# Kernel tuning notes

Measured on AMD Instinct MI355X. Metric: run time of the kernel, lower is better.

Reference implementation:

```python
import jax, jax.numpy as jnp
import numpy as np

N, C, H, O, NUM_CLASSES = 4096, 768, 512, 50, 1


def setup_inputs() -> dict:
    key = jax.random.key(0)
    ks = jax.random.split(key, 8)
    x = jax.random.normal(ks[0], (N, C), dtype=jnp.float32)
    labels = jax.random.randint(ks[1], (N,), 0, 2, dtype=jnp.int64)
    W1 = jax.random.normal(ks[2], (C, H), dtype=jnp.float32) / np.sqrt(C)
    b1 = jnp.zeros((H,), dtype=jnp.float32)
    W2 = jax.random.normal(ks[3], (H, O), dtype=jnp.float32) / np.sqrt(H)
    b2 = jnp.zeros((O,), dtype=jnp.float32)
    fcW = jax.random.normal(ks[4], (C + O, NUM_CLASSES), dtype=jnp.float32) / np.sqrt(C + O)
    fcb = jnp.zeros((NUM_CLASSES,), dtype=jnp.float32)
    return {"x": x, "labels": labels, "W1": W1, "b1": b1, "W2": W2, "b2": b2, "fcW": fcW, "fcb": fcb}


def _build_graph(x, labels):
    # similarity-threshold edge construction (dense masked form of the python double loop)
    sim = x @ x.T                                   # [N, N]
    n = x.shape[0]
    diff = labels[:, None] != labels[None, :]       # cross-label pairs
    cnt = jnp.sum(diff)
    s = jnp.sum(jnp.where(diff, sim, 0.0))
    threshold = jnp.where(cnt > 0, s / cnt.astype(sim.dtype), jnp.asarray(0.0, sim.dtype))
    eye = jnp.eye(n, dtype=bool)
    same = (labels[:, None] == labels[None, :]) & ~eye
    edge_mask = same & (sim <= threshold)           # symmetric (sim symmetric)
    loss_mask = edge_mask & (jnp.arange(n)[:, None] < jnp.arange(n)[None, :])  # i<j pairs
    adj = jax.lax.stop_gradient(edge_mask.astype(x.dtype))
    # GCN normalization with self-loops
    a = adj + jnp.eye(n, dtype=x.dtype)
    dinv = jax.lax.rsqrt(jnp.sum(a, axis=1))        # deg >= 1
    norm_adj = dinv[:, None] * a * dinv[None, :]
    return norm_adj, loss_mask


def reference(x, labels, W1, b1, W2, b2, fcW, fcb):
    norm_adj, loss_mask = _build_graph(x, labels)
    h = jax.nn.relu(norm_adj @ (x @ W1) + b1)       # conv1 + relu
    g = norm_adj @ (h @ W2) + b2                    # conv2
    f_g = jnp.concatenate([x, g], axis=-1)          # [N, C+O]
    out = f_g @ fcW + fcb                           # [N, 1]
    return out, f_g, loss_mask, x
```

## Files before the change

### kernel.cpp

```cpp
#include <hip/hip_runtime.h>
#include <hip/hip_bf16.h>
#include <math.h>

#define NN 4096
#define CD 768
#define HD 512
#define OD 50
#define FGD 818

typedef short short8 __attribute__((ext_vector_type(8)));
typedef float f32x4 __attribute__((ext_vector_type(4)));
typedef unsigned short us4 __attribute__((ext_vector_type(4)));
typedef unsigned short ushortT;
typedef unsigned char uchar;
typedef unsigned long long u64;

__device__ inline ushortT f2bf(float v) {
    __hip_bfloat16 b = __float2bfloat16(v);
    return *(ushortT*)&b;
}
__device__ inline float bf2f(ushortT u) {
    __hip_bfloat16 b = *(__hip_bfloat16*)&u;
    return __bfloat162float(b);
}
__device__ inline float dinv_of(int d) {
    return (float)(1.0 / sqrt((double)(1 + d)));
}

__global__ __launch_bounds__(256) void gsum_kernel(const float* __restrict__ x,
                                                   const int* __restrict__ labels,
                                                   double* __restrict__ gsum) {
    int b = blockIdx.x;
    int t = threadIdx.x;
    double a0[3] = {0, 0, 0}, a1[3] = {0, 0, 0};
    for (int rr = 0; rr < 16; ++rr) {
        int row = b * 16 + rr;
        int lab = labels[row];
#pragma unroll
        for (int s = 0; s < 3; ++s) {
            double v = (double)x[(size_t)row * CD + t + s * 256];
            if (lab == 0) a0[s] += v; else a1[s] += v;
        }
    }
#pragma unroll
    for (int s = 0; s < 3; ++s) {
        atomicAdd(&gsum[t + s * 256], a0[s]);
        atomicAdd(&gsum[768 + t + s * 256], a1[s]);
    }
}

__global__ __launch_bounds__(256) void gdot_kernel(const double* __restrict__ gsum,
                                                   const int* __restrict__ labels,
                                                   double* __restrict__ scal) {
    int t = threadIdx.x;
    double d = 0.0;
    for (int c = t; c < CD; c += 256) d += gsum[c] * gsum[768 + c];
    int n0 = 0;
    for (int i = t; i < NN; i += 256) n0 += (labels[i] == 0) ? 1 : 0;
    for (int off = 32; off; off >>= 1) {
        d += __shfl_down(d, off);
        n0 += __shfl_down(n0, off);
    }
    __shared__ double sd[4];
    __shared__ int sn[4];
    int wid = t >> 6, lane = t & 63;
    if (lane == 0) { sd[wid] = d; sn[wid] = n0; }
    __syncthreads();
    if (t == 0) {
        double D = sd[0] + sd[1] + sd[2] + sd[3];
        double N0 = (double)(sn[0] + sn[1] + sn[2] + sn[3]);
        scal[0] = 2.0 * D;
        scal[1] = 2.0 * N0 * ((double)NN - N0);
    }
}

#define BAND 4e-3
#define RC_CAP (1 << 18)

__global__ __launch_bounds__(256) void sim_fused(
    const ushortT* __restrict__ xh, const ushortT* __restrict__ xl,
    const int* __restrict__ labels, const double* __restrict__ scal,
    u64* __restrict__ abbits, float* __restrict__ lm, int* __restrict__ deg,
    int* __restrict__ rc_cnt, int* __restrict__ rc_list) {
    int t = blockIdx.x;
    int by = (int)((129.0 - sqrt(16641.0 - 8.0 * (double)t)) * 0.5);
    while (by * (129 - by) / 2 > t) --by;
    while ((by + 1) * (129 - (by + 1)) / 2 <= t) ++by;
    int bx = by + (t - by * (129 - by) / 2);
    bool diag = (bx == by);

    __shared__ ushortT lds[4 * 64 * 72];
    __shared__ int larr[128];
    int tid = threadIdx.x;
    int lane = tid & 63;
    int w = tid >> 6;
    int wr = w >> 1, wc = w & 1;
    int m = lane & 15, quad = lane >> 4;
    int row0 = by * 64, col0 = bx * 64;

    if (tid < 64) larr[tid] = labels[row0 + tid];
    else if (tid < 128) larr[tid] = labels[col0 + tid - 64];

    f32x4 acc[2][2] = {{{0.f, 0.f, 0.f, 0.f}, {0.f, 0.f, 0.f, 0.f}},
                       {{0.f, 0.f, 0.f, 0.f}, {0.f, 0.f, 0.f, 0.f}}};

    for (int k0 = 0; k0 < CD; k0 += 64) {
#pragma unroll
        for (int tt = 0; tt < 2; ++tt) {
            int id2 = tid + tt * 256;
            int row = id2 >> 3, c8 = (id2 & 7) * 8;
            *(short8*)&lds[0 * 4608 + row * 72 + c8] =
                *(const short8*)&xh[(size_t)(row0 + row) * CD + k0 + c8];
            *(short8*)&lds[1 * 4608 + row * 72 + c8] =
                *(const short8*)&xl[(size_t)(row0 + row) * CD + k0 + c8];
            *(short8*)&lds[2 * 4608 + row * 72 + c8] =
                *(const short8*)&xh[(size_t)(col0 + row) * CD + k0 + c8];
            *(short8*)&lds[3 * 4608 + row * 72 + c8] =
                *(const short8*)&xl[(size_t)(col0 + row) * CD + k0 + c8];
        }
        __syncthreads();
#pragma unroll
        for (int ks = 0; ks < 2; ++ks) {
            short8 ah[2], al[2], bh[2], bl[2];
#pragma unroll
            for (int i = 0; i < 2; ++i) {
                int ro = (wr * 32 + i * 16 + m) * 72 + ks * 32 + quad * 8;
                ah[i] = *(const short8*)&lds[0 * 4608 + ro];
                al[i] = *(const short8*)&lds[1 * 4608 + ro];
            }
#pragma unroll
            for (int j = 0; j < 2; ++j) {
                int co = (wc * 32 + j * 16 + m) * 72 + ks * 32 + quad * 8;
                bh[j] = *(const short8*)&lds[2 * 4608 + co];
                bl[j] = *(const short8*)&lds[3 * 4608 + co];
            }
#pragma unroll
            for (int i = 0; i < 2; ++i)
#pragma unroll
                for (int j = 0; j < 2; ++j) {
                    acc[i][j] = __builtin_amdgcn_mfma_f32_16x16x32_bf16(
                        ah[i], bh[j], acc[i][j], 0, 0, 0);
                    acc[i][j] = __builtin_amdgcn_mfma_f32_16x16x32_bf16(
                        ah[i], bl[j], acc[i][j], 0, 0, 0);
                    acc[i][j] = __builtin_amdgcn_mfma_f32_16x16x32_bf16(
                        al[i], bh[j], acc[i][j], 0, 0, 0);
                }
        }
        __syncthreads();
    }

    double thrd;
    {
        double cnt = scal[1];
        thrd = (cnt > 0.0) ? (scal[0] / cnt) : 0.0;
    }
    uchar* flags = (uchar*)lds;
#pragma unroll
    for (int i = 0; i < 2; ++i)
#pragma unroll
        for (int j = 0; j < 2; ++j) {
#pragma unroll
            for (int r = 0; r < 4; ++r) {
                int row = wr * 32 + i * 16 + quad * 4 + r;
                int col = wc * 32 + j * 16 + m;
                bool same = (larr[row] == larr[64 + col]);
                bool selfp = ((row0 + row) == (col0 + col));
                bool edge = false;
                if (same && !selfp) {
                    double s = (double)acc[i][j][r];
                    if (s <= thrd - BAND) {
                        edge = true;
                    } else if (s <= thrd + BAND) {
                        edge = (s <= thrd);
                        int enc = ((row0 + row) << 12) | (col0 + col) |
                                  (diag ? 0 : (1 << 24)) |
                                  (edge ? (1 << 25) : 0);
                        int idx = atomicAdd(rc_cnt, 1);
                        if (idx < RC_CAP) rc_list[idx] = enc;
                    }
                }
                flags[row * 68 + col] = edge ? 1 : 0;
            }
        }
    __syncthreads();

    {
        int r = tid >> 2, q = tid & 3;
        int cnti = 0;
        unsigned int bits16 = 0;
#pragma unroll
        for (int s = 0; s < 4; ++s) {
            int cb = q * 16 + s * 4;
            float4 f;
#pragma unroll
            for (int k2 = 0; k2 < 4; ++k2) {
                int c = cb + k2;
                bool fl = flags[r * 68 + c] != 0;
                cnti += fl ? 1 : 0;
                if (fl || (diag && r == c)) bits16 |= 1u << (s * 4 + k2);
                ((float*)&f)[k2] = (fl && (row0 + r < col0 + c)) ? 1.0f : 0.0f;
            }
            *(float4*)&lm[(size_t)(row0 + r) * NN + col0 + cb] = f;
        }
        unsigned int s1 = __shfl_down(bits16, 1);
        unsigned int s2 = __shfl_down(bits16, 2);
        unsigned int s3 = __shfl_down(bits16, 3);
        cnti += __shfl_down(cnti, 1);
        cnti += __shfl_down(cnti, 2);
        if (q == 0) {
            u64 u = (u64)bits16 | ((u64)s1 << 16) | ((u64)s2 << 32) |
                    ((u64)s3 << 48);
            abbits[(size_t)(row0 + r) * 64 + bx] = u;
            if (cnti) atomicAdd(&deg[row0 + r], cnti);
        }
    }

    if (!diag) {
        int c = tid >> 2, q = tid & 3;
        int cnti = 0;
        unsigned int bits16 = 0;
        float4 fz = {0.0f, 0.0f, 0.0f, 0.0f};
#pragma unroll
        for (int s = 0; s < 4; ++s) {
            int rb = q * 16 + s * 4;
#pragma unroll
            for (int k2 = 0; k2 < 4; ++k2) {
                bool fl = flags[(rb + k2) * 68 + c] != 0;
                cnti += fl ? 1 : 0;
                if (fl) bits16 |= 1u << (s * 4 + k2);
            }
            *(float4*)&lm[(size_t)(col0 + c) * NN + row0 + rb] = fz;
        }
        unsigned int s1 = __shfl_down(bits16, 1);
        unsigned int s2 = __shfl_down(bits16, 2);
        unsigned int s3 = __shfl_down(bits16, 3);
        cnti += __shfl_down(cnti, 1);
        cnti += __shfl_down(cnti, 2);
        if (q == 0) {
            u64 u = (u64)bits16 | ((u64)s1 << 16) | ((u64)s2 << 32) |
                    ((u64)s3 << 48);
            abbits[(size_t)(col0 + c) * 64 + by] = u;
            if (cnti) atomicAdd(&deg[col0 + c], cnti);
        }
    }
}

__global__ __launch_bounds__(256) void rc_fix(
    const float* __restrict__ x, const double* __restrict__ scal,
    const int* __restrict__ rc_cnt, const int* __restrict__ rc_list,
    u64* __restrict__ abbits, float* __restrict__ lm, int* __restrict__ deg) {
    int cnt = *rc_cnt;
    if (cnt > RC_CAP) cnt = RC_CAP;
    double thrd;
    {
        double c = scal[1];
        thrd = (c > 0.0) ? (scal[0] / c) : 0.0;
    }
    int lane = threadIdx.x & 63;
    int wid = (blockIdx.x * 256 + threadIdx.x) >> 6;
    int nw = (gridDim.x * 256) >> 6;
    for (int e = wid; e < cnt; e += nw) {
        int enc = rc_list[e];
        int c = enc & 0xFFF;
        int r = (enc >> 12) & 0xFFF;
        bool mirror = (enc >> 24) & 1;
        bool prov = (enc >> 25) & 1;
        const float* xi = x + (size_t)r * CD;
        const float* xj = x + (size_t)c * CD;
        double d = 0.0;
#pragma unroll
        for (int s = 0; s < 12; ++s)
            d += (double)xi[lane + s * 64] * (double)xj[lane + s * 64];
        for (int off = 32; off; off >>= 1) d += __shfl_down(d, off);
        if (lane == 0) {
            bool exact = (d <= thrd);
            if (exact != prov) {
                u64 mk = 1ull << (c & 63);
                if (exact) atomicOr(&abbits[(size_t)r * 64 + (c >> 6)], mk);
                else       atomicAnd(&abbits[(size_t)r * 64 + (c >> 6)], ~mk);
                lm[(size_t)r * NN + c] = (exact && r < c) ? 1.0f : 0.0f;
                int dlt = exact ? 1 : -1;
                atomicAdd(&deg[r], dlt);
                if (mirror) {
                    u64 mk2 = 1ull << (r & 63);
                    if (exact) atomicOr(&abbits[(size_t)c * 64 + (r >> 6)], mk2);
                    else       atomicAnd(&abbits[(size_t)c * 64 + (r >> 6)], ~mk2);
                    atomicAdd(&deg[c], dlt);
                }
            }
        }
    }
}

__global__ __launch_bounds__(256) void prep_kernel(
    const float* __restrict__ x, const float* __restrict__ W1,
    const float* __restrict__ W2, float* __restrict__ fg, float* __restrict__ xo,
    ushortT* __restrict__ xh, ushortT* __restrict__ xl, ushortT* __restrict__ w1t,
    ushortT* __restrict__ w2t) {
    int b = blockIdx.x;
    if (b < 4096) {
        int t = threadIdx.x;
        if (t < 192) {
            float4 v = *(const float4*)&x[(size_t)b * CD + t * 4];
            *(float4*)&xo[(size_t)b * CD + t * 4] = v;
            fg[(size_t)b * FGD + t * 4 + 0] = v.x;
            fg[(size_t)b * FGD + t * 4 + 1] = v.y;
            fg[(size_t)b * FGD + t * 4 + 2] = v.z;
            fg[(size_t)b * FGD + t * 4 + 3] = v.w;
            us4 hh, ll;
            float* vp = (float*)&v;
#pragma unroll
            for (int k = 0; k < 4; ++k) {
                ushortT h = f2bf(vp[k]);
                ((ushortT*)&hh)[k] = h;
                ((ushortT*)&ll)[k] = f2bf(vp[k] - bf2f(h));
            }
            *(us4*)&xh[(size_t)b * CD + t * 4] = hh;
            *(us4*)&xl[(size_t)b * CD + t * 4] = ll;
        }
        return;
    }
    __shared__ float tT[32][33];
    const float* P;
    ushortT* T;
    int K, N, Npad, k0, n0;
    if (b < 4480) {
        int bb = b - 4096;
        P = W1; T = w1t; K = CD; N = HD; Npad = HD;
        k0 = (bb % 24) * 32; n0 = (bb / 24) * 32;
    } else {
        int bb = b - 4480;
        P = W2; T = w2t; K = HD; N = OD; Npad = 64;
        k0 = (bb % 16) * 32; n0 = (bb / 16) * 32;
    }
    int tx = threadIdx.x & 31, ty = threadIdx.x >> 5;
#pragma unroll
    for (int s = 0; s < 4; ++s) {
        int k = k0 + ty + s * 8, n = n0 + tx;
        tT[ty + s * 8][tx] = (k < K && n < N) ? P[(size_t)k * N + n] : 0.0f;
    }
    __syncthreads();
#pragma unroll
    for (int s = 0; s < 4; ++s) {
        int n = n0 + ty + s * 8, k = k0 + tx;
        if (n < Npad && k < K) T[(size_t)n * K + k] = f2bf(tT[tx][ty + s * 8]);
    }
}

template <bool RELU, bool HASBIAS, int EPI>
__global__ __launch_bounds__(256) void gemm_bf16(
    const ushortT* __restrict__ A, const ushortT* __restrict__ B,
    ushortT* __restrict__ Cb, int M, int Nn, int K, int ldc,
    const int* __restrict__ deg, const float* __restrict__ bias) {
    __shared__ ushortT lds[2 * 64 * 72];
    int tid = threadIdx.x;
    int lane = tid & 63;
    int w = tid >> 6;
    int wr = w >> 1, wc = w & 1;
    int m = lane & 15, quad = lane >> 4;
    int row0 = blockIdx.y * 64, col0 = blockIdx.x * 64;

    f32x4 acc[2][2] = {{{0.f, 0.f, 0.f, 0.f}, {0.f, 0.f, 0.f, 0.f}},
                       {{0.f, 0.f, 0.f, 0.f}, {0.f, 0.f, 0.f, 0.f}}};

    for (int k0 = 0; k0 < K; k0 += 64) {
#pragma unroll
        for (int t = 0; t < 2; ++t) {
            int id2 = tid + t * 256;
            int row = id2 >> 3, c8 = (id2 & 7) * 8;
            *(short8*)&lds[row * 72 + c8] =
                *(const short8*)&A[(size_t)(row0 + row) * K + k0 + c8];
            *(short8*)&lds[4608 + row * 72 + c8] =
                *(const short8*)&B[(size_t)(col0 + row) * K + k0 + c8];
        }
        __syncthreads();
#pragma unroll
        for (int ks = 0; ks < 2; ++ks) {
            short8 af[2], bf[2];
#pragma unroll
            for (int i = 0; i < 2; ++i)
                af[i] = *(const short8*)&lds[(wr * 32 + i * 16 + m) * 72 +
                                             ks * 32 + quad * 8];
#pragma unroll
            for (int j = 0; j < 2; ++j)
                bf[j] = *(const short8*)&lds[4608 + (wc * 32 + j * 16 + m) * 72 +
                                             ks * 32 + quad * 8];
#pragma unroll
            for (int i = 0; i < 2; ++i)
#pragma unroll
                for (int j = 0; j < 2; ++j)
                    acc[i][j] = __builtin_amdgcn_mfma_f32_16x16x32_bf16(
                        af[i], bf[j], acc[i][j], 0, 0, 0);
        }
        __syncthreads();
    }

    if (EPI == 2) {
        ushortT* Th = lds;
#pragma unroll
        for (int i = 0; i < 2; ++i)
#pragma unroll
            for (int j = 0; j < 2; ++j)
#pragma unroll
                for (int r = 0; r < 4; ++r) {
                    int row = wr * 32 + i * 16 + quad * 4 + r;
                    int col = wc * 32 + j * 16 + m;
                    float dv = dinv_of(deg[row0 + row]);
                    Th[col * 72 + row] = f2bf(acc[i][j][r] * dv);
                }
        __syncthreads();
#pragma unroll
        for (int t = 0; t < 2; ++t) {
            int id2 = tid + t * 256;
            int cc = id2 >> 3, chunk = id2 & 7;
            *(short8*)&Cb[(size_t)(col0 + cc) * M + row0 + chunk * 8] =
                *(const short8*)&Th[cc * 72 + chunk * 8];
        }
    } else {
#pragma unroll
        for (int i = 0; i < 2; ++i)
#pragma unroll
            for (int j = 0; j < 2; ++j)
#pragma unroll
                for (int r = 0; r < 4; ++r) {
                    int row = wr * 32 + i * 16 + quad * 4 + r;
                    int col = wc * 32 + j * 16 + m;
                    int gr = row0 + row, gc = col0 + col;
                    if (gc < Nn) {
                        float v = acc[i][j][r] * dinv_of(deg[gr]);
                        if (HASBIAS) v += bias[gc];
                        if (RELU) v = fmaxf(v, 0.0f);
                        Cb[(size_t)gr * ldc + gc] = f2bf(v);
                    }
                }
    }
}

__global__ __launch_bounds__(256) void gemm_part(
    const ushortT* __restrict__ A, const ushortT* __restrict__ B,
    float* __restrict__ P, int M, int K, int KC) {
    __shared__ ushortT lds[2 * 64 * 72];
    int tid = threadIdx.x;
    int lane = tid & 63;
    int w = tid >> 6;
    int wr = w >> 1, wc = w & 1;
    int m = lane & 15, quad = lane >> 4;
    int kb = blockIdx.x;
    int row0 = blockIdx.y * 64;
    int kbase = kb * KC;

    f32x4 acc[2][2] = {{{0.f, 0.f, 0.f, 0.f}, {0.f, 0.f, 0.f, 0.f}},
                       {{0.f, 0.f, 0.f, 0.f}, {0.f, 0.f, 0.f, 0.f}}};

    for (int k0 = 0; k0 < KC; k0 += 64) {
#pragma unroll
        for (int t = 0; t < 2; ++t) {
            int id2 = tid + t * 256;
            int row = id2 >> 3, c8 = (id2 & 7) * 8;
            *(short8*)&lds[row * 72 + c8] =
                *(const short8*)&A[(size_t)(row0 + row) * K + kbase + k0 + c8];
            *(short8*)&lds[4608 + row * 72 + c8] =
                *(const short8*)&B[(size_t)row * K + kbase + k0 + c8];
        }
        __syncthreads();
#pragma unroll
        for (int ks = 0; ks < 2; ++ks) {
            short8 af[2], bf[2];
#pragma unroll
            for (int i = 0; i < 2; ++i)
                af[i] = *(const short8*)&lds[(wr * 32 + i * 16 + m) * 72 +
                                             ks * 32 + quad * 8];
#pragma unroll
            for (int j = 0; j < 2; ++j)
                bf[j] = *(const short8*)&lds[4608 + (wc * 32 + j * 16 + m) * 72 +
                                             ks * 32 + quad * 8];
#pragma unroll
            for (int i = 0; i < 2; ++i)
#pragma unroll
                for (int j = 0; j < 2; ++j)
                    acc[i][j] = __builtin_amdgcn_mfma_f32_16x16x32_bf16(
                        af[i], bf[j], acc[i][j], 0, 0, 0);
        }
        __syncthreads();
    }
#pragma unroll
    for (int i = 0; i < 2; ++i)
#pragma unroll
        for (int j = 0; j < 2; ++j)
#pragma unroll
            for (int r = 0; r < 4; ++r) {
                int row = wr * 32 + i * 16 + quad * 4 + r;
                int col = wc * 32 + j * 16 + m;
                P[((size_t)kb * M + row0 + row) * 64 + col] = acc[i][j][r];
            }
}

__global__ __launch_bounds__(256) void gemm_partB(
    const u64* __restrict__ Abits, const ushortT* __restrict__ B,
    float* __restrict__ P, int M, int K, int KC) {
    __shared__ ushortT lds[2 * 64 * 72];
    int tid = threadIdx.x;
    int lane = tid & 63;
    int w = tid >> 6;
    int wr = w >> 1, wc = w & 1;
    int m = lane & 15, quad = lane >> 4;
    int kb = blockIdx.x;
    int row0 = blockIdx.y * 64;
    int kbase = kb * KC;
    int er = tid >> 2, eq = tid & 3;

    f32x4 acc[2][2] = {{{0.f, 0.f, 0.f, 0.f}, {0.f, 0.f, 0.f, 0.f}},
                       {{0.f, 0.f, 0.f, 0.f}, {0.f, 0.f, 0.f, 0.f}}};

    for (int k0 = 0; k0 < KC; k0 += 64) {
#pragma unroll
        for (int t = 0; t < 2; ++t) {
            int id2 = tid + t * 256;
            int row = id2 >> 3, c8 = (id2 & 7) * 8;
            *(short8*)&lds[4608 + row * 72 + c8] =
                *(const short8*)&B[(size_t)row * K + kbase + k0 + c8];
        }
        {
            u64 bits = Abits[(size_t)(row0 + er) * 64 + ((kbase + k0) >> 6)];
            unsigned int half = (unsigned int)(bits >> (eq * 16)) & 0xFFFFu;
            short8 v0, v1;
#pragma unroll
            for (int k = 0; k < 8; ++k) {
                ((ushortT*)&v0)[k] =
                    ((half >> k) & 1) ? (ushortT)0x3F80 : (ushortT)0;
                ((ushortT*)&v1)[k] =
                    ((half >> (k + 8)) & 1) ? (ushortT)0x3F80 : (ushortT)0;
            }
            *(short8*)&lds[er * 72 + eq * 16] = v0;
            *(short8*)&lds[er * 72 + eq * 16 + 8] = v1;
        }
        __syncthreads();
#pragma unroll
        for (int ks = 0; ks < 2; ++ks) {
            short8 af[2], bf[2];
#pragma unroll
            for (int i = 0; i < 2; ++i)
                af[i] = *(const short8*)&lds[(wr * 32 + i * 16 + m) * 72 +
                                             ks * 32 + quad * 8];
#pragma unroll
            for (int j = 0; j < 2; ++j)
                bf[j] = *(const short8*)&lds[4608 + (wc * 32 + j * 16 + m) * 72 +
                                             ks * 32 + quad * 8];
#pragma unroll
            for (int i = 0; i < 2; ++i)
#pragma unroll
                for (int j = 0; j < 2; ++j)
                    acc[i][j] = __builtin_amdgcn_mfma_f32_16x16x32_bf16(
                        af[i], bf[j], acc[i][j], 0, 0, 0);
        }
        __syncthreads();
    }
#pragma unroll
    for (int i = 0; i < 2; ++i)
#pragma unroll
        for (int j = 0; j < 2; ++j)
#pragma unroll
            for (int r = 0; r < 4; ++r) {
                int row = wr * 32 + i * 16 + quad * 4 + r;
                int col = wc * 32 + j * 16 + m;
                P[((size_t)kb * M + row0 + row) * 64 + col] = acc[i][j][r];
            }
}

__global__ __launch_bounds__(256) void gemm_partWB(
    const u64* __restrict__ Abits, const ushortT* __restrict__ B,
    float* __restrict__ P, int M, int K, int KC, int ldP) {
    __shared__ ushortT lds[2 * 64 * 72];
    int tid = threadIdx.x;
    int lane = tid & 63;
    int w = tid >> 6;
    int wr = w >> 1, wc = w & 1;
    int m = lane & 15, quad = lane >> 4;
    int col0 = blockIdx.x * 64;
    int row0 = blockIdx.y * 64;
    int kb = blockIdx.z;
    int kbase = kb * KC;
    int er = tid >> 2, eq = tid & 3;

    f32x4 acc[2][2] = {{{0.f, 0.f, 0.f, 0.f}, {0.f, 0.f, 0.f, 0.f}},
                       {{0.f, 0.f, 0.f, 0.f}, {0.f, 0.f, 0.f, 0.f}}};

    for (int k0 = 0; k0 < KC; k0 += 64) {
#pragma unroll
        for (int t = 0; t < 2; ++t) {
            int id2 = tid + t * 256;
            int row = id2 >> 3, c8 = (id2 & 7) * 8;
            *(short8*)&lds[4608 + row * 72 + c8] =
                *(const short8*)&B[(size_t)(col0 + row) * K + kbase + k0 + c8];
        }
        {
            u64 bits = Abits[(size_t)(row0 + er) * 64 + ((kbase + k0) >> 6)];
            unsigned int half = (unsigned int)(bits >> (eq * 16)) & 0xFFFFu;
            short8 v0, v1;
#pragma unroll
            for (int k = 0; k < 8; ++k) {
                ((ushortT*)&v0)[k] =
                    ((half >> k) & 1) ? (ushortT)0x3F80 : (ushortT)0;
                ((ushortT*)&v1)[k] =
                    ((half >> (k + 8)) & 1) ? (ushortT)0x3F80 : (ushortT)0;
            }
            *(short8*)&lds[er * 72 + eq * 16] = v0;
            *(short8*)&lds[er * 72 + eq * 16 + 8] = v1;
        }
        __syncthreads();
#pragma unroll
        for (int ks = 0; ks < 2; ++ks) {
            short8 af[2], bf[2];
#pragma unroll
            for (int i = 0; i < 2; ++i)
                af[i] = *(const short8*)&lds[(wr * 32 + i * 16 + m) * 72 +
                                             ks * 32 + quad * 8];
#pragma unroll
            for (int j = 0; j < 2; ++j)
                bf[j] = *(const short8*)&lds[4608 + (wc * 32 + j * 16 + m) * 72 +
                                             ks * 32 + quad * 8];
#pragma unroll
            for (int i = 0; i < 2; ++i)
#pragma unroll
                for (int j = 0; j < 2; ++j)
                    acc[i][j] = __builtin_amdgcn_mfma_f32_16x16x32_bf16(
                        af[i], bf[j], acc[i][j], 0, 0, 0);
        }
        __syncthreads();
    }
#pragma unroll
    for (int i = 0; i < 2; ++i)
#pragma unroll
        for (int j = 0; j < 2; ++j)
#pragma unroll
            for (int r = 0; r < 4; ++r) {
                int row = wr * 32 + i * 16 + quad * 4 + r;
                int col = wc * 32 + j * 16 + m;
                P[((size_t)kb * M + row0 + row) * ldP + col0 + col] =
                    acc[i][j][r];
            }
}

__global__ __launch_bounds__(256) void k5_epi(const float* __restrict__ P5,
                                              const int* __restrict__ deg,
                                              const float* __restrict__ b1,
                                              ushortT* __restrict__ hb) {
    int tid = threadIdx.x;
    int cg = tid & 127;
    int rr = tid >> 7;
#pragma unroll
    for (int p = 0; p < 2; ++p) {
        int r = blockIdx.x * 4 + p * 2 + rr;
        float dv = dinv_of(deg[r]);
        float4 s = {0.f, 0.f, 0.f, 0.f};
#pragma unroll
        for (int kb = 0; kb < 4; ++kb) {
            float4 v = *(const float4*)&P5[((size_t)kb * NN + r) * HD + cg * 4];
            s.x += v.x; s.y += v.y; s.z += v.z; s.w += v.w;
        }
        float4 bv = *(const float4*)&b1[cg * 4];
        us4 o;
        o[0] = f2bf(fmaxf(s.x * dv + bv.x, 0.f));
        o[1] = f2bf(fmaxf(s.y * dv + bv.y, 0.f));
        o[2] = f2bf(fmaxf(s.z * dv + bv.z, 0.f));
        o[3] = f2bf(fmaxf(s.w * dv + bv.w, 0.f));
        *(us4*)&hb[(size_t)r * HD + cg * 4] = o;
    }
}

__global__ __launch_bounds__(256) void k6_epi(const float* __restrict__ P6,
                                              const int* __restrict__ deg,
                                              ushortT* __restrict__ hw2sT) {
    __shared__ ushortT Th[64 * 72];
    int row0 = blockIdx.x * 64;
    int tid = threadIdx.x;
    int rl = tid >> 2, q = tid & 3;
    float dv = dinv_of(deg[row0 + rl]);
#pragma unroll
    for (int s = 0; s < 16; ++s) {
        int c = q * 16 + s;
        float v = 0.f;
#pragma unroll
        for (int kb = 0; kb < 4; ++kb)
            v += P6[((size_t)kb * NN + row0 + rl) * 64 + c];
        Th[c * 72 + rl] = f2bf(v * dv);
    }
    __syncthreads();
#pragma unroll
    for (int t = 0; t < 2; ++t) {
        int id2 = tid + t * 256;
        int cc = id2 >> 3, chunk = id2 & 7;
        *(short8*)&hw2sT[(size_t)cc * NN + row0 + chunk * 8] =
            *(const short8*)&Th[cc * 72 + chunk * 8];
    }
}

__global__ __launch_bounds__(256) void k7_epi_out(
    const float* __restrict__ P7, const int* __restrict__ deg,
    const float* __restrict__ b2, const float* __restrict__ fcW,
    const float* __restrict__ fcb, float* __restrict__ fg,
    float* __restrict__ out) {
    int row0 = blockIdx.x * 64;
    int tid = threadIdx.x;
    int rl = tid >> 2, q = tid & 3;
    int r = row0 + rl;
    float dv = dinv_of(deg[r]);
    float sg = 0.f;
#pragma unroll
    for (int s = 0; s < 16; ++s) {
        int c = q * 16 + s;
        if (c < OD) {
            float v = 0.f;
#pragma unroll
            for (int kb = 0; kb < 8; ++kb)
                v += P7[((size_t)kb * NN + r) * 64 + c];
            v = v * dv + b2[c];
            fg[(size_t)r * FGD + CD + c] = v;
            sg += v * fcW[CD + c];
        }
    }
    const float* fr = fg + (size_t)r * FGD;
    float sx = 0.f;
    for (int k = q * 192; k < (q + 1) * 192; k += 2) {
        float2 vv = *(const float2*)&fr[k];
        float2 ww = *(const float2*)&fcW[k];
        sx += vv.x * ww.x + vv.y * ww.y;
    }
    float s = sx + sg;
    s += __shfl_down(s, 1);
    s += __shfl_down(s, 2);
    if (q == 0) out[r] = s + fcb[0];
}

extern "C" void kernel_launch(void* const* d_in, const int* in_sizes, int n_in,
                              void* d_out, int out_size, void* d_ws, size_t ws_size,
                              hipStream_t stream) {
    const float* x = (const float*)d_in[0];
    const int* labels = (const int*)d_in[1];
    const float* W1 = (const float*)d_in[2];
    const float* b1 = (const float*)d_in[3];
    const float* W2 = (const float*)d_in[4];
    const float* b2 = (const float*)d_in[5];
    const float* fcW = (const float*)d_in[6];
    const float* fcb = (const float*)d_in[7];
    float* outp = (float*)d_out;

    const size_t o_out = 0;
    const size_t o_fg = 4096;
    const size_t o_lm = o_fg + (size_t)NN * FGD;
    const size_t o_x = o_lm + (size_t)NN * NN;

    char* ws = (char*)d_ws;
    size_t off = 0;
    u64* abbits = (u64*)(ws + off); off += (size_t)NN * 64 * 8;
    ushortT* xh = (ushortT*)(ws + off); off += (size_t)NN * CD * 2;
    ushortT* xl = (ushortT*)(ws + off); off += (size_t)NN * CD * 2;
    ushortT* w1t = (ushortT*)(ws + off); off += (size_t)HD * CD * 2;
    ushortT* xw1sT = (ushortT*)(ws + off); off += (size_t)HD * NN * 2;
    ushortT* hb = (ushortT*)(ws + off); off += (size_t)NN * HD * 2;
    ushortT* w2t = (ushortT*)(ws + off); off += (size_t)64 * HD * 2;
    ushortT* hw2sT = (ushortT*)(ws + off); off += (size_t)64 * NN * 2;
    char* zbase = ws + off;
    int* deg = (int*)(ws + off); off += (size_t)NN * 4;
    double* gsum = (double*)(ws + off); off += 1536 * 8;
    double* scal = (double*)(ws + off); off += 16;
    int* rc_cnt = (int*)(ws + off); off += 16;
    size_t zbytes = (size_t)NN * 4 + 1536 * 8 + 16 + 16;
    char* uni = ws + off;
    int* rc_list = (int*)uni;
    float* P5 = (float*)uni;
    float* P6 = (float*)uni;
    float* P7 = (float*)uni;
    off += (size_t)4 * NN * HD * 4;

    hipMemsetAsync(zbase, 0, zbytes, stream);

    prep_kernel<<<4512, 256, 0, stream>>>(x, W1, W2, outp + o_fg, outp + o_x, xh, xl,
                                          w1t, w2t);

    gsum_kernel<<<256, 256, 0, stream>>>(x, labels, gsum);
    gdot_kernel<<<1, 256, 0, stream>>>(gsum, labels, scal);

    sim_fused<<<2080, 256, 0, stream>>>(xh, xl, labels, scal, abbits, outp + o_lm,
                                        deg, rc_cnt, rc_list);

    rc_fix<<<512, 256, 0, stream>>>(x, scal, rc_cnt, rc_list, abbits, outp + o_lm,
                                    deg);

    gemm_bf16<false, false, 2><<<dim3(HD / 64, NN / 64), 256, 0, stream>>>(
        xh, w1t, xw1sT, NN, HD, CD, 0, deg, nullptr);

    gemm_partWB<<<dim3(HD / 64, NN / 64, 4), 256, 0, stream>>>(
        abbits, xw1sT, P5, NN, NN, NN / 4, HD);
    k5_epi<<<NN / 4, 256, 0, stream>>>(P5, deg, b1, hb);

    gemm_part<<<dim3(4, NN / 64), 256, 0, stream>>>(hb, w2t, P6, NN, HD, HD / 4);
    k6_epi<<<NN / 64, 256, 0, stream>>>(P6, deg, hw2sT);

    gemm_partB<<<dim3(8, NN / 64), 256, 0, stream>>>(abbits, hw2sT, P7, NN, NN,
                                                     NN / 8);
    k7_epi_out<<<NN / 64, 256, 0, stream>>>(P7, deg, b2, fcW, fcb, outp + o_fg,
                                            outp + o_out);
}
```

Baseline: 332.9 us.

## Prefetch next K-tile into registers and swizzle block order for L2 reuse

```diff
diff --git a/kernel.cpp b/kernel.cpp
--- a/kernel.cpp
+++ b/kernel.cpp
@@ -82,11 +82,27 @@
     const int* __restrict__ labels, const double* __restrict__ scal,
     u64* __restrict__ abbits, float* __restrict__ lm, int* __restrict__ deg,
     int* __restrict__ rc_cnt, int* __restrict__ rc_list) {
-    int t = blockIdx.x;
-    int by = (int)((129.0 - sqrt(16641.0 - 8.0 * (double)t)) * 0.5);
-    while (by * (129 - by) / 2 > t) --by;
-    while ((by + 1) * (129 - (by + 1)) / 2 <= t) ++by;
-    int bx = by + (t - by * (129 - by) / 2);
+    int bid = blockIdx.x;
+    int sid = (bid & 7) * 260 + (bid >> 3);
+    int sby = 0, rem = sid;
+    for (; sby < 8; ++sby) {
+        int rowsz = 36 + (7 - sby) * 64;
+        if (rem < rowsz) break;
+        rem -= rowsz;
+    }
+    int sbx, iby, ibx;
+    if (rem < 36) {
+        sbx = sby;
+        iby = 0;
+        while (rem >= 8 - iby) { rem -= 8 - iby; ++iby; }
+        ibx = iby + rem;
+    } else {
+        rem -= 36;
+        sbx = sby + 1 + (rem >> 6);
+        int u = rem & 63;
+        iby = u >> 3; ibx = u & 7;
+    }
+    int by = sby * 8 + iby, bx = sbx * 8 + ibx;
     bool diag = (bx == by);
 
     __shared__ ushortT lds[4 * 64 * 72];
@@ -104,21 +120,42 @@
     f32x4 acc[2][2] = {{{0.f, 0.f, 0.f, 0.f}, {0.f, 0.f, 0.f, 0.f}},
                        {{0.f, 0.f, 0.f, 0.f}, {0.f, 0.f, 0.f, 0.f}}};
 
+    const size_t rowbase = (size_t)row0 * CD;
+    const size_t colbase = (size_t)col0 * CD;
+    short8 rg[2][4];
+#pragma unroll
+    for (int tt = 0; tt < 2; ++tt) {
+        int id2 = tid + tt * 256;
+        int row = id2 >> 3, c8 = (id2 & 7) * 8;
+        rg[tt][0] = *(const short8*)&xh[rowbase + (size_t)row * CD + c8];
+        rg[tt][1] = *(const short8*)&xl[rowbase + (size_t)row * CD + c8];
+        rg[tt][2] = *(const short8*)&xh[colbase + (size_t)row * CD + c8];
+        rg[tt][3] = *(const short8*)&xl[colbase + (size_t)row * CD + c8];
+    }
+
     for (int k0 = 0; k0 < CD; k0 += 64) {
+        __syncthreads();
 #pragma unroll
         for (int tt = 0; tt < 2; ++tt) {
             int id2 = tid + tt * 256;
             int row = id2 >> 3, c8 = (id2 & 7) * 8;
-            *(short8*)&lds[0 * 4608 + row * 72 + c8] =
-                *(const short8*)&xh[(size_t)(row0 + row) * CD + k0 + c8];
-            *(short8*)&lds[1 * 4608 + row * 72 + c8] =
-                *(const short8*)&xl[(size_t)(row0 + row) * CD + k0 + c8];
-            *(short8*)&lds[2 * 4608 + row * 72 + c8] =
-                *(const short8*)&xh[(size_t)(col0 + row) * CD + k0 + c8];
-            *(short8*)&lds[3 * 4608 + row * 72 + c8] =
-                *(const short8*)&xl[(size_t)(col0 + row) * CD + k0 + c8];
-        }
-        __syncthreads();
+            *(short8*)&lds[0 * 4608 + row * 72 + c8] = rg[tt][0];
+            *(short8*)&lds[1 * 4608 + row * 72 + c8] = rg[tt][1];
+            *(short8*)&lds[2 * 4608 + row * 72 + c8] = rg[tt][2];
+            *(short8*)&lds[3 * 4608 + row * 72 + c8] = rg[tt][3];
+        }
+        __syncthreads();
+        if (k0 + 64 < CD) {
+#pragma unroll
+            for (int tt = 0; tt < 2; ++tt) {
+                int id2 = tid + tt * 256;
+                int row = id2 >> 3, c8 = (id2 & 7) * 8 + k0 + 64;
+                rg[tt][0] = *(const short8*)&xh[rowbase + (size_t)row * CD + c8];
+                rg[tt][1] = *(const short8*)&xl[rowbase + (size_t)row * CD + c8];
+                rg[tt][2] = *(const short8*)&xh[colbase + (size_t)row * CD + c8];
+                rg[tt][3] = *(const short8*)&xl[colbase + (size_t)row * CD + c8];
+            }
+        }
 #pragma unroll
         for (int ks = 0; ks < 2; ++ks) {
             short8 ah[2], al[2], bh[2], bl[2];
@@ -146,8 +183,8 @@
                         al[i], bh[j], acc[i][j], 0, 0, 0);
                 }
         }
-        __syncthreads();
-    }
+    }
+    __syncthreads();
 
     double thrd;
     {
```

After: 322.2 us. -3.2%, faster.
